# Optimization experiments

Measured on AMD Instinct MI355X. Metric: run time of the kernel, lower is better.

## Reference

```python
import jax, jax.numpy as jnp
import numpy as np

N_FREQ = 7  # freqs = 2**linspace(0, 6, 7) == 2**arange(7)
SKIP = (4,)


def nerf_encode(p):
    # nerfstudio NeRFEncoding with include_input=True, windows_param=None
    freqs = 2.0 ** jnp.arange(N_FREQ, dtype=p.dtype)          # [7]
    scaled = (2.0 * jnp.pi) * p                               # [N,3]
    s = (scaled[..., None] * freqs).reshape(p.shape[0], -1)   # [N,21]
    enc = jnp.sin(jnp.concatenate([s, s + 0.5 * jnp.pi], axis=-1))  # [N,42] = sin | cos
    return jnp.concatenate([enc, p], axis=-1)                 # [N,45]


def _hat_pt3d(w):
    # pytorch3d hat convention (transpose of the standard skew matrix)
    x, y, z = w[:, 0], w[:, 1], w[:, 2]
    o = jnp.zeros_like(x)
    return jnp.stack([
        jnp.stack([o, z, -y], -1),
        jnp.stack([-z, o, x], -1),
        jnp.stack([y, -x, o], -1)], -2)                       # [N,3,3]


def se3_exp_map_T(screw, eps=1e-4):
    # pytorch3d.transforms.se3_exp_map(screw).permute(0, 2, 1)
    v, w = screw[:, :3], screw[:, 3:]
    ang2 = jnp.clip(jnp.sum(w * w, axis=-1), eps, None)
    ang = jnp.sqrt(ang2)
    K = _hat_pt3d(w)
    KK = jnp.matmul(K, K)
    f1 = (jnp.sin(ang) / ang)[:, None, None]
    f2 = ((1.0 - jnp.cos(ang)) / ang2)[:, None, None]
    f3 = ((ang - jnp.sin(ang)) / (ang * ang2))[:, None, None]
    I = jnp.eye(3, dtype=screw.dtype)
    R = I + f1 * K + f2 * KK       # pytorch3d (row-vector) rotation
    V = I + f2 * K + f3 * KK
    T = jnp.einsum('nij,nj->ni', V, v)
    M = jnp.zeros((screw.shape[0], 4, 4), screw.dtype)
    M = M.at[:, :3, :3].set(jnp.swapaxes(R, -1, -2))  # transpose of [[R,0],[T,1]]
    M = M.at[:, :3, 3].set(T)
    M = M.at[:, 3, 3].set(1.0)
    return M


def mlp_stem(x, Ws, bs):
    inp = x
    n = len(Ws)
    for i in range(n):
        if i in SKIP:
            x = jnp.concatenate([inp, x], axis=-1)
        x = x @ Ws[i].T + bs[i]
        x = jax.nn.relu(x)  # hidden activation; i==n-1 is out_activation (also ReLU)
    return x


def setup_inputs() -> dict:
    key = jax.random.key(0)
    ks = jax.random.split(key, 16)
    N = 524288
    d = {
        'positions': jax.random.uniform(ks[0], (N, 3), jnp.float32),
        'directions': jax.random.normal(ks[1], (N, 3), jnp.float32),
        'warp_code': jax.random.normal(ks[2], (N, 8), jnp.float32),
    }
    fan_ins = [53, 128, 128, 128, 181, 128]
    for i, fi in enumerate(fan_ins):
        d[f'W{i}'] = jax.random.normal(ks[3 + i], (128, fi), jnp.float32) / np.sqrt(fi)
        d[f'b{i}'] = jnp.zeros((128,), jnp.float32)
    d['Wr'] = jax.random.normal(ks[10], (3, 128), jnp.float32) * 1e-5
    d['br'] = jnp.zeros((3,), jnp.float32)
    d['Wv'] = jax.random.normal(ks[11], (3, 128), jnp.float32) * 1e-5
    d['bv'] = jnp.zeros((3,), jnp.float32)
    return d


def reference(positions, directions, warp_code,
              W0, b0, W1, b1, W2, b2, W3, b3, W4, b4, W5, b5,
              Wr, br, Wv, bv):
    enc = nerf_encode(positions)                                  # [N,45]
    feat = mlp_stem(jnp.concatenate([enc, warp_code], axis=-1),
                    [W0, W1, W2, W3, W4, W5], [b0, b1, b2, b3, b4, b5])  # [N,128]
    r = feat @ Wr.T + br                                          # [N,3]
    v = feat @ Wv.T + bv                                          # [N,3]
    screw = jnp.concatenate([v, r], axis=-1)                      # [N,6]
    M = se3_exp_map_T(screw)                                      # [N,4,4]
    ph = jnp.concatenate([positions, jnp.ones_like(positions[:, :1])], axis=-1)
    wp_h = jnp.einsum('nij,nj->ni', M, ph)                        # [N,4]
    wp = wp_h[:, :3] / wp_h[:, 3:]
    wp = jnp.where(jnp.isnan(wp), positions, wp)
    rots = M[:, :3, :3]
    wd = jnp.einsum('nij,nj->ni', rots, directions)
    wd = jnp.where(jnp.isnan(wd), directions, wd)
    return wp, wd
```

## Files before the change

kernel.cpp:

```cpp
#include <hip/hip_runtime.h>
#include <hip/hip_bf16.h>
#include <math.h>


typedef __bf16 bf16x8 __attribute__((ext_vector_type(8)));
typedef float  f32x4  __attribute__((ext_vector_type(4)));

#define NROWS 524288
#define BROWS 128

#define P0 0
#define P1 8192
#define P2 24576
#define P3 40960
#define P4 57344
#define P5 81920
#define PH 98304
#define PTOT 100352

#define X0_OFF 0
#define XA_OFF 16384
#define SC_OFF 0
#define LDS_SZ 49152

__global__ void pack_w(const float* __restrict__ W0, const float* __restrict__ W1,
                       const float* __restrict__ W2, const float* __restrict__ W3,
                       const float* __restrict__ W4, const float* __restrict__ W5,
                       const float* __restrict__ Wr, const float* __restrict__ Wv,
                       __bf16* __restrict__ pk)
{
    int e = blockIdx.x * 256 + threadIdx.x;
    if (e >= PTOT) return;
    float val = 0.f;
    if (e >= PH) {
        int rem = e - PH;
        int s = rem >> 9, r3 = rem & 511, ln = r3 >> 3, j = r3 & 7;
        int col = ln & 15;
        int k = s * 32 + (ln >> 4) * 8 + j;
        if (col < 3)      val = Wv[col * 128 + k];
        else if (col < 6) val = Wr[(col - 3) * 128 + k];
        else              val = 0.f;
    } else {
        const float* W; int KS, base, fan;
        if (e < P1)      { W = W0; KS = 2; base = P0; fan = 53;  }
        else if (e < P2) { W = W1; KS = 4; base = P1; fan = 128; }
        else if (e < P3) { W = W2; KS = 4; base = P2; fan = 128; }
        else if (e < P4) { W = W3; KS = 4; base = P3; fan = 128; }
        else if (e < P5) { W = W4; KS = 6; base = P4; fan = 181; }
        else             { W = W5; KS = 4; base = P5; fan = 128; }
        int rem = e - base;
        int perf = KS * 512;
        int f = rem / perf, r2 = rem % perf;
        int s = r2 >> 9, r3 = r2 & 511, ln = r3 >> 3, j = r3 & 7;
        int col = f * 16 + (ln & 15);
        int k = s * 32 + (ln >> 4) * 8 + j;
        if (fan == 128)     val = W[col * 128 + k];
        else if (fan == 53) val = (k < 53) ? W[col * 53 + k] : 0.f;
        else {
            if (k < 53)      val = W[col * 181 + k];
            else if (k < 64) val = 0.f;
            else             val = W[col * 181 + (k - 11)];
        }
    }
    pk[e] = (__bf16)val;
}

__device__ __forceinline__ unsigned pack_bf16_2(float a, float b) {
    union { __bf16 h; unsigned short u; } x, y;
    x.h = (__bf16)a; y.h = (__bf16)b;
    return ((unsigned)y.u << 16) | (unsigned)x.u;
}

template<int KS, int SPLITS>
__device__ __forceinline__ void mlp_layer(unsigned char* smem,
    const __bf16* __restrict__ pkL, const float* __restrict__ bias,
    int inOff, int inStride, int outOff,
    int lane, int cl, int gp, int mfG, int nfG)
{
    const bf16x8* pW = (const bf16x8*)pkL;

    f32x4 acc[4][4];
    #pragma unroll
    for (int mf = 0; mf < 4; mf++) {
        f32x4 bb = *(const f32x4*)(bias + mfG * 64 + mf * 16 + gp * 4);
        #pragma unroll
        for (int nf = 0; nf < 4; nf++) acc[mf][nf] = bb;
    }

    bf16x8 Wf[2][4], Bf[2][4];
    auto loadW = [&](bf16x8* dst, int s) {
        #pragma unroll
        for (int mf = 0; mf < 4; mf++)
            dst[mf] = pW[((mfG * 4 + mf) * KS + s) * 64 + lane];
    };
    auto loadB = [&](bf16x8* dst, int s) {
        int base, stride, k0;
        if (s < SPLITS) { base = X0_OFF; stride = 128;      k0 = s * 32; }
        else            { base = inOff;  stride = inStride; k0 = (s - SPLITS) * 32; }
        int bc = 2 * k0 + 16 * gp;
        #pragma unroll
        for (int nf = 0; nf < 4; nf++) {
            int row = nfG * 64 + nf * 16 + cl;
            dst[nf] = *(const bf16x8*)(smem + base + row * stride
                                       + (bc ^ ((row & 7) << 4)));
        }
    };

    loadW(Wf[0], 0);
    loadB(Bf[0], 0);
    #pragma unroll
    for (int s = 0; s < KS; s++) {
        if (s + 1 < KS) { loadW(Wf[(s + 1) & 1], s + 1); loadB(Bf[(s + 1) & 1], s + 1); }
        #pragma unroll
        for (int mf = 0; mf < 4; mf++)
            #pragma unroll
            for (int nf = 0; nf < 4; nf++)
                acc[mf][nf] = __builtin_amdgcn_mfma_f32_16x16x32_bf16(
                    Wf[s & 1][mf], Bf[s & 1][nf], acc[mf][nf], 0, 0, 0);
    }

    __syncthreads();
    #pragma unroll
    for (int mf = 0; mf < 4; mf++)
        #pragma unroll
        for (int nf = 0; nf < 4; nf++) {
            int row = nfG * 64 + nf * 16 + cl;
            int bc  = 128 * mfG + 32 * mf + 8 * gp;
            f32x4 a = acc[mf][nf];
            uint2 w;
            w.x = pack_bf16_2(fmaxf(a[0], 0.f), fmaxf(a[1], 0.f));
            w.y = pack_bf16_2(fmaxf(a[2], 0.f), fmaxf(a[3], 0.f));
            *(uint2*)(smem + outOff + row * 256 + (bc ^ ((row & 7) << 4))) = w;
        }
    __syncthreads();
}

__global__ __launch_bounds__(256, 3)
void se3_fused(const float* __restrict__ pos, const float* __restrict__ dir,
               const float* __restrict__ wcode,
               const float* __restrict__ b0, const float* __restrict__ b1,
               const float* __restrict__ b2, const float* __restrict__ b3,
               const float* __restrict__ b4, const float* __restrict__ b5,
               const float* __restrict__ br, const float* __restrict__ bv,
               const __bf16* __restrict__ pk,
               float* __restrict__ out)
{
    __shared__ unsigned char smem[LDS_SZ];
    const int tid  = threadIdx.x;
    const int lane = tid & 63;
    const int cl   = lane & 15;
    const int gp   = lane >> 4;
    const int wid  = tid >> 6;
    const int mfG  = wid & 1;
    const int nfG  = wid >> 1;
    const int r0   = blockIdx.x * BROWS;

    {
        int row = tid >> 1, h = tid & 1;
        int g = r0 + row;
        float p3[3] = { pos[g*3+0], pos[g*3+1], pos[g*3+2] };
        unsigned char* base = smem + X0_OFF + row * 128;
        int sw = (row & 7) << 4;
        auto put = [&](int col, float v) {
            *(__bf16*)(base + ((col * 2) ^ sw)) = (__bf16)v;
        };
        if (h == 0) {
            #pragma unroll
            for (int a = 0; a < 3; a++)
                #pragma unroll
                for (int f = 0; f < 4; f++) {
                    float t = p3[a] * (float)(1 << f);
                    t -= floorf(t);
                    float ang = 6.283185307179586f * t;
                    put(a*7+f,      __sinf(ang));
                    put(21+a*7+f,   __cosf(ang));
                }
        } else {
            #pragma unroll
            for (int a = 0; a < 3; a++)
                #pragma unroll
                for (int f = 4; f < 7; f++) {
                    float t = p3[a] * (float)(1 << f);
                    t -= floorf(t);
                    float ang = 6.283185307179586f * t;
                    put(a*7+f,      __sinf(ang));
                    put(21+a*7+f,   __cosf(ang));
                }
            put(42, p3[0]); put(43, p3[1]); put(44, p3[2]);
            #pragma unroll
            for (int j = 0; j < 8; j++) put(45+j, wcode[g*8+j]);
            #pragma unroll
            for (int c = 53; c < 64; c++) put(c, 0.f);
        }
    }
    __syncthreads();

    mlp_layer<2,0>(smem, pk + P0, b0, X0_OFF, 128, XA_OFF, lane, cl, gp, mfG, nfG);
    mlp_layer<4,0>(smem, pk + P1, b1, XA_OFF, 256, XA_OFF, lane, cl, gp, mfG, nfG);
    mlp_layer<4,0>(smem, pk + P2, b2, XA_OFF, 256, XA_OFF, lane, cl, gp, mfG, nfG);
    mlp_layer<4,0>(smem, pk + P3, b3, XA_OFF, 256, XA_OFF, lane, cl, gp, mfG, nfG);
    mlp_layer<6,2>(smem, pk + P4, b4, XA_OFF, 256, XA_OFF, lane, cl, gp, mfG, nfG);
    mlp_layer<4,0>(smem, pk + P5, b5, XA_OFF, 256, XA_OFF, lane, cl, gp, mfG, nfG);

    if (mfG == 0) {
        const bf16x8* pW = (const bf16x8*)(pk + PH);
        f32x4 hb;
        #pragma unroll
        for (int r = 0; r < 4; r++) {
            int m = gp * 4 + r;
            hb[r] = (m < 3) ? bv[m] : ((m < 6) ? br[m - 3] : 0.f);
        }
        f32x4 hacc[4];
        #pragma unroll
        for (int nf = 0; nf < 4; nf++) hacc[nf] = hb;
        #pragma unroll
        for (int s = 0; s < 4; s++) {
            bf16x8 Wh = pW[s * 64 + lane];
            int bc = 64 * s + 16 * gp;
            #pragma unroll
            for (int nf = 0; nf < 4; nf++) {
                int row = nfG * 64 + nf * 16 + cl;
                bf16x8 B = *(const bf16x8*)(smem + XA_OFF + row * 256
                                            + (bc ^ ((row & 7) << 4)));
                hacc[nf] = __builtin_amdgcn_mfma_f32_16x16x32_bf16(Wh, B, hacc[nf], 0, 0, 0);
            }
        }
        #pragma unroll
        for (int nf = 0; nf < 4; nf++) {
            int row = nfG * 64 + nf * 16 + cl;
            if (gp == 0) {
                *(f32x4*)(smem + SC_OFF + row * 32) = hacc[nf];
            } else if (gp == 1) {
                *(float*)(smem + SC_OFF + row * 32 + 16) = hacc[nf][0];
                *(float*)(smem + SC_OFF + row * 32 + 20) = hacc[nf][1];
            }
        }
    }
    __syncthreads();

    if (tid < BROWS) {
        int row = tid, g = r0 + row;
        const float* sc = (const float*)(smem + SC_OFF + row * 32);
        float v0 = sc[0], v1 = sc[1], v2 = sc[2];
        float wx = sc[3], wy = sc[4], wz = sc[5];
        float ang2 = wx*wx + wy*wy + wz*wz;
        ang2 = fmaxf(ang2, 1e-4f);
        float ang = sqrtf(ang2);
        float sn = __sinf(ang), cs = __cosf(ang);
        float f1 = sn / ang;
        float f2 = (1.f - cs) / ang2;
        float f3 = (ang - sn) / (ang * ang2);
        float K[3][3] = {{0.f,  wz, -wy}, {-wz, 0.f,  wx}, { wy, -wx, 0.f}};
        float KK[3][3];
        #pragma unroll
        for (int i = 0; i < 3; i++)
            #pragma unroll
            for (int j = 0; j < 3; j++)
                KK[i][j] = K[i][0]*K[0][j] + K[i][1]*K[1][j] + K[i][2]*K[2][j];
        float R[3][3], V[3][3];
        #pragma unroll
        for (int i = 0; i < 3; i++)
            #pragma unroll
            for (int j = 0; j < 3; j++) {
                float id = (i == j) ? 1.f : 0.f;
                R[i][j] = id + f1 * K[i][j] + f2 * KK[i][j];
                V[i][j] = id + f2 * K[i][j] + f3 * KK[i][j];
            }
        float T0 = V[0][0]*v0 + V[0][1]*v1 + V[0][2]*v2;
        float T1 = V[1][0]*v0 + V[1][1]*v1 + V[1][2]*v2;
        float T2 = V[2][0]*v0 + V[2][1]*v1 + V[2][2]*v2;
        float px = pos[g*3+0], py = pos[g*3+1], pz = pos[g*3+2];
        float dx = dir[g*3+0], dy = dir[g*3+1], dz = dir[g*3+2];
        float wpx = R[0][0]*px + R[1][0]*py + R[2][0]*pz + T0;
        float wpy = R[0][1]*px + R[1][1]*py + R[2][1]*pz + T1;
        float wpz = R[0][2]*px + R[1][2]*py + R[2][2]*pz + T2;
        float wdx = R[0][0]*dx + R[1][0]*dy + R[2][0]*dz;
        float wdy = R[0][1]*dx + R[1][1]*dy + R[2][1]*dz;
        float wdz = R[0][2]*dx + R[1][2]*dy + R[2][2]*dz;
        wpx = (wpx != wpx) ? px : wpx;
        wpy = (wpy != wpy) ? py : wpy;
        wpz = (wpz != wpz) ? pz : wpz;
        wdx = (wdx != wdx) ? dx : wdx;
        wdy = (wdy != wdy) ? dy : wdy;
        wdz = (wdz != wdz) ? dz : wdz;
        out[g*3+0] = wpx; out[g*3+1] = wpy; out[g*3+2] = wpz;
        float* o2 = out + (size_t)NROWS * 3;
        o2[g*3+0] = wdx; o2[g*3+1] = wdy; o2[g*3+2] = wdz;
    }
}

extern "C" void kernel_launch(void* const* d_in, const int* in_sizes, int n_in,
                              void* d_out, int out_size, void* d_ws, size_t ws_size,
                              hipStream_t stream)
{
    const float* pos = (const float*)d_in[0];
    const float* dir = (const float*)d_in[1];
    const float* wc  = (const float*)d_in[2];
    const float* W0 = (const float*)d_in[3];  const float* b0 = (const float*)d_in[4];
    const float* W1 = (const float*)d_in[5];  const float* b1 = (const float*)d_in[6];
    const float* W2 = (const float*)d_in[7];  const float* b2 = (const float*)d_in[8];
    const float* W3 = (const float*)d_in[9];  const float* b3 = (const float*)d_in[10];
    const float* W4 = (const float*)d_in[11]; const float* b4 = (const float*)d_in[12];
    const float* W5 = (const float*)d_in[13]; const float* b5 = (const float*)d_in[14];
    const float* Wr = (const float*)d_in[15]; const float* br = (const float*)d_in[16];
    const float* Wv = (const float*)d_in[17]; const float* bv = (const float*)d_in[18];
    __bf16* pk = (__bf16*)d_ws;
    float* out = (float*)d_out;

    pack_w<<<(PTOT + 255) / 256, 256, 0, stream>>>(W0, W1, W2, W3, W4, W5, Wr, Wv, pk);
    se3_fused<<<NROWS / BROWS, 256, 0, stream>>>(pos, dir, wc,
                                                 b0, b1, b2, b3, b4, b5,
                                                 br, bv, pk, out);
}
```

Baseline: 221.9 us.

## Prefetch next layer's weights and bias into registers across MLP layers

Weights and bias for the next MLP layer are now loaded from global memory into a persistent register array during the epilogue of the current layer, so their latency overlaps the LDS writeback and barrier instead of stalling the start of each layer. The input encoding now builds bf16 values in registers and writes them as packed 16-byte LDS stores, and the final barrier only waits on LDS traffic (lgkmcnt) so outstanding global prefetches are not drained. The weight-packing kernel is restructured with templated helpers, and the head weights are hoisted. Holding a 4x4 bf16x8 weight array raises register pressure and may hurt occupancy under the 3-blocks launch bound.

```diff
diff --git a/kernel.cpp b/kernel.cpp
--- a/kernel.cpp
+++ b/kernel.cpp
@@ -23,6 +23,21 @@
 #define SC_OFF 0
 #define LDS_SZ 49152
 
+template<int KS, int FAN>
+__device__ __forceinline__ float pack_val(const float* __restrict__ W, int idx)
+{
+    int f  = idx / (KS * 512);
+    int r2 = idx % (KS * 512);
+    int s  = r2 >> 9, r3 = r2 & 511, ln = r3 >> 3, j = r3 & 7;
+    int col = f * 16 + (ln & 15);
+    int k   = s * 32 + (ln >> 4) * 8 + j;
+    if (FAN == 128) return W[col * 128 + k];
+    if (FAN == 53)  return (k < 53) ? W[col * 53 + k] : 0.f;
+    if (k < 53)  return W[col * 181 + k];
+    if (k < 64)  return 0.f;
+    return W[col * 181 + (k - 11)];
+}
+
 __global__ void pack_w(const float* __restrict__ W0, const float* __restrict__ W1,
                        const float* __restrict__ W2, const float* __restrict__ W3,
                        const float* __restrict__ W4, const float* __restrict__ W5,
@@ -31,7 +46,7 @@
 {
     int e = blockIdx.x * 256 + threadIdx.x;
     if (e >= PTOT) return;
-    float val = 0.f;
+    float val;
     if (e >= PH) {
         int rem = e - PH;
         int s = rem >> 9, r3 = rem & 511, ln = r3 >> 3, j = r3 & 7;
@@ -40,28 +55,13 @@
         if (col < 3)      val = Wv[col * 128 + k];
         else if (col < 6) val = Wr[(col - 3) * 128 + k];
         else              val = 0.f;
-    } else {
-        const float* W; int KS, base, fan;
-        if (e < P1)      { W = W0; KS = 2; base = P0; fan = 53;  }
-        else if (e < P2) { W = W1; KS = 4; base = P1; fan = 128; }
-        else if (e < P3) { W = W2; KS = 4; base = P2; fan = 128; }
-        else if (e < P4) { W = W3; KS = 4; base = P3; fan = 128; }
-        else if (e < P5) { W = W4; KS = 6; base = P4; fan = 181; }
-        else             { W = W5; KS = 4; base = P5; fan = 128; }
-        int rem = e - base;
-        int perf = KS * 512;
-        int f = rem / perf, r2 = rem % perf;
-        int s = r2 >> 9, r3 = r2 & 511, ln = r3 >> 3, j = r3 & 7;
-        int col = f * 16 + (ln & 15);
-        int k = s * 32 + (ln >> 4) * 8 + j;
-        if (fan == 128)     val = W[col * 128 + k];
-        else if (fan == 53) val = (k < 53) ? W[col * 53 + k] : 0.f;
-        else {
-            if (k < 53)      val = W[col * 181 + k];
-            else if (k < 64) val = 0.f;
-            else             val = W[col * 181 + (k - 11)];
-        }
-    }
+    }
+    else if (e < P1) val = pack_val<2, 53 >(W0, e - P0);
+    else if (e < P2) val = pack_val<4, 128>(W1, e - P1);
+    else if (e < P3) val = pack_val<4, 128>(W2, e - P2);
+    else if (e < P4) val = pack_val<4, 128>(W3, e - P3);
+    else if (e < P5) val = pack_val<6, 181>(W4, e - P4);
+    else             val = pack_val<4, 128>(W5, e - P5);
     pk[e] = (__bf16)val;
 }
 
@@ -71,28 +71,21 @@
     return ((unsigned)y.u << 16) | (unsigned)x.u;
 }
 
-template<int KS, int SPLITS>
+template<int KS, int SPLITS, int KSN>
 __device__ __forceinline__ void mlp_layer(unsigned char* smem,
-    const __bf16* __restrict__ pkL, const float* __restrict__ bias,
+    bf16x8 (&W)[4][4], f32x4 (&Bias)[4],
+    const __bf16* __restrict__ pkCur, const __bf16* __restrict__ pkNext,
+    const float* __restrict__ biasNext,
     int inOff, int inStride, int outOff,
     int lane, int cl, int gp, int mfG, int nfG)
 {
-    const bf16x8* pW = (const bf16x8*)pkL;
-
     f32x4 acc[4][4];
     #pragma unroll
-    for (int mf = 0; mf < 4; mf++) {
-        f32x4 bb = *(const f32x4*)(bias + mfG * 64 + mf * 16 + gp * 4);
-        #pragma unroll
-        for (int nf = 0; nf < 4; nf++) acc[mf][nf] = bb;
-    }
-
-    bf16x8 Wf[2][4], Bf[2][4];
-    auto loadW = [&](bf16x8* dst, int s) {
-        #pragma unroll
-        for (int mf = 0; mf < 4; mf++)
-            dst[mf] = pW[((mfG * 4 + mf) * KS + s) * 64 + lane];
-    };
+    for (int mf = 0; mf < 4; mf++)
+        #pragma unroll
+        for (int nf = 0; nf < 4; nf++) acc[mf][nf] = Bias[mf];
+
+    bf16x8 Bf[2][4];
     auto loadB = [&](bf16x8* dst, int s) {
         int base, stride, k0;
         if (s < SPLITS) { base = X0_OFF; stride = 128;      k0 = s * 32; }
@@ -106,20 +99,41 @@
         }
     };
 
-    loadW(Wf[0], 0);
     loadB(Bf[0], 0);
     #pragma unroll
     for (int s = 0; s < KS; s++) {
-        if (s + 1 < KS) { loadW(Wf[(s + 1) & 1], s + 1); loadB(Bf[(s + 1) & 1], s + 1); }
+        if (s + 1 < KS) loadB(Bf[(s + 1) & 1], s + 1);
         #pragma unroll
         for (int mf = 0; mf < 4; mf++)
             #pragma unroll
             for (int nf = 0; nf < 4; nf++)
                 acc[mf][nf] = __builtin_amdgcn_mfma_f32_16x16x32_bf16(
-                    Wf[s & 1][mf], Bf[s & 1][nf], acc[mf][nf], 0, 0, 0);
+                    W[s & 3][mf], Bf[s & 1][nf], acc[mf][nf], 0, 0, 0);
+        if constexpr (KS > 4) {
+            if (s + 4 < KS) {
+                const bf16x8* pC = (const bf16x8*)pkCur;
+                #pragma unroll
+                for (int mf = 0; mf < 4; mf++)
+                    W[(s + 4) & 3][mf] = pC[((mfG * 4 + mf) * KS + (s + 4)) * 64 + lane];
+            }
+        }
     }
 
     __syncthreads();
+
+    if constexpr (KSN > 0) {
+        constexpr int PF = (KSN > 4) ? 4 : KSN;
+        const bf16x8* pN = (const bf16x8*)pkNext;
+        #pragma unroll
+        for (int s = 0; s < PF; s++)
+            #pragma unroll
+            for (int mf = 0; mf < 4; mf++)
+                W[s][mf] = pN[((mfG * 4 + mf) * KSN + s) * 64 + lane];
+        #pragma unroll
+        for (int mf = 0; mf < 4; mf++)
+            Bias[mf] = *(const f32x4*)(biasNext + mfG * 64 + mf * 16 + gp * 4);
+    }
+
     #pragma unroll
     for (int mf = 0; mf < 4; mf++)
         #pragma unroll
@@ -132,7 +146,10 @@
             w.y = pack_bf16_2(fmaxf(a[2], 0.f), fmaxf(a[3], 0.f));
             *(uint2*)(smem + outOff + row * 256 + (bc ^ ((row & 7) << 4))) = w;
         }
-    __syncthreads();
+
+    asm volatile("s_waitcnt lgkmcnt(0)" ::: "memory");
+    __builtin_amdgcn_s_barrier();
+    asm volatile("" ::: "memory");
 }
 
 __global__ __launch_bounds__(256, 3)
@@ -155,55 +172,83 @@
     const int nfG  = wid >> 1;
     const int r0   = blockIdx.x * BROWS;
 
+    bf16x8 W[4][4];
+    f32x4  Bias[4];
+    {
+        const bf16x8* p0v = (const bf16x8*)(pk + P0);
+        #pragma unroll
+        for (int s = 0; s < 2; s++)
+            #pragma unroll
+            for (int mf = 0; mf < 4; mf++)
+                W[s][mf] = p0v[((mfG * 4 + mf) * 2 + s) * 64 + lane];
+        #pragma unroll
+        for (int mf = 0; mf < 4; mf++)
+            Bias[mf] = *(const f32x4*)(b0 + mfG * 64 + mf * 16 + gp * 4);
+    }
+
     {
         int row = tid >> 1, h = tid & 1;
         int g = r0 + row;
-        float p3[3] = { pos[g*3+0], pos[g*3+1], pos[g*3+2] };
+        float p0 = pos[g*3+0], p1 = pos[g*3+1], p2 = pos[g*3+2];
+        float vals[32];
+        if (h == 0) {
+            #pragma unroll
+            for (int j = 0; j < 21; j++) {
+                float p = (j < 7) ? p0 : (j < 14 ? p1 : p2);
+                float t = p * (float)(1 << (j % 7));
+                t -= floorf(t);
+                vals[j] = __sinf(6.283185307179586f * t);
+            }
+            #pragma unroll
+            for (int j = 21; j < 32; j++) {
+                int idx = j - 21;
+                float p = (idx < 7) ? p0 : (idx < 14 ? p1 : p2);
+                float t = p * (float)(1 << (idx % 7));
+                t -= floorf(t);
+                vals[j] = __cosf(6.283185307179586f * t);
+            }
+        } else {
+            #pragma unroll
+            for (int j = 0; j < 10; j++) {
+                int idx = 11 + j;
+                float p = (idx < 14) ? p1 : p2;
+                float t = p * (float)(1 << (idx % 7));
+                t -= floorf(t);
+                vals[j] = __cosf(6.283185307179586f * t);
+            }
+            vals[10] = p0; vals[11] = p1; vals[12] = p2;
+            const float4* wc4 = (const float4*)(wcode + (size_t)g * 8);
+            float4 wa = wc4[0], wb = wc4[1];
+            vals[13] = wa.x; vals[14] = wa.y; vals[15] = wa.z; vals[16] = wa.w;
+            vals[17] = wb.x; vals[18] = wb.y; vals[19] = wb.z; vals[20] = wb.w;
+            #pragma unroll
+            for (int j = 21; j < 32; j++) vals[j] = 0.f;
+        }
+        unsigned pkd[16];
+        #pragma unroll
+        for (int i = 0; i < 16; i++) pkd[i] = pack_bf16_2(vals[2*i], vals[2*i+1]);
         unsigned char* base = smem + X0_OFF + row * 128;
         int sw = (row & 7) << 4;
-        auto put = [&](int col, float v) {
-            *(__bf16*)(base + ((col * 2) ^ sw)) = (__bf16)v;
-        };
-        if (h == 0) {
-            #pragma unroll
-            for (int a = 0; a < 3; a++)
-                #pragma unroll
-                for (int f = 0; f < 4; f++) {
-                    float t = p3[a] * (float)(1 << f);
-                    t -= floorf(t);
-                    float ang = 6.283185307179586f * t;
-                    put(a*7+f,      __sinf(ang));
-                    put(21+a*7+f,   __cosf(ang));
-                }
-        } else {
-            #pragma unroll
-            for (int a = 0; a < 3; a++)
-                #pragma unroll
-                for (int f = 4; f < 7; f++) {
-                    float t = p3[a] * (float)(1 << f);
-                    t -= floorf(t);
-                    float ang = 6.283185307179586f * t;
-                    put(a*7+f,      __sinf(ang));
-                    put(21+a*7+f,   __cosf(ang));
-                }
-            put(42, p3[0]); put(43, p3[1]); put(44, p3[2]);
-            #pragma unroll
-            for (int j = 0; j < 8; j++) put(45+j, wcode[g*8+j]);
-            #pragma unroll
-            for (int c = 53; c < 64; c++) put(c, 0.f);
+        #pragma unroll
+        for (int c = 0; c < 4; c++) {
+            uint4 w; w.x = pkd[4*c]; w.y = pkd[4*c+1]; w.z = pkd[4*c+2]; w.w = pkd[4*c+3];
+            *(uint4*)(base + ((64 * h + 16 * c) ^ sw)) = w;
         }
     }
     __syncthreads();
 
-    mlp_layer<2,0>(smem, pk + P0, b0, X0_OFF, 128, XA_OFF, lane, cl, gp, mfG, nfG);
-    mlp_layer<4,0>(smem, pk + P1, b1, XA_OFF, 256, XA_OFF, lane, cl, gp, mfG, nfG);
-    mlp_layer<4,0>(smem, pk + P2, b2, XA_OFF, 256, XA_OFF, lane, cl, gp, mfG, nfG);
-    mlp_layer<4,0>(smem, pk + P3, b3, XA_OFF, 256, XA_OFF, lane, cl, gp, mfG, nfG);
-    mlp_layer<6,2>(smem, pk + P4, b4, XA_OFF, 256, XA_OFF, lane, cl, gp, mfG, nfG);
-    mlp_layer<4,0>(smem, pk + P5, b5, XA_OFF, 256, XA_OFF, lane, cl, gp, mfG, nfG);
+    mlp_layer<2,0,4>(smem, W, Bias, pk+P0, pk+P1, b1, X0_OFF, 128, XA_OFF, lane, cl, gp, mfG, nfG);
+    mlp_layer<4,0,4>(smem, W, Bias, pk+P1, pk+P2, b2, XA_OFF, 256, XA_OFF, lane, cl, gp, mfG, nfG);
+    mlp_layer<4,0,4>(smem, W, Bias, pk+P2, pk+P3, b3, XA_OFF, 256, XA_OFF, lane, cl, gp, mfG, nfG);
+    mlp_layer<4,0,6>(smem, W, Bias, pk+P3, pk+P4, b4, XA_OFF, 256, XA_OFF, lane, cl, gp, mfG, nfG);
+    mlp_layer<6,2,4>(smem, W, Bias, pk+P4, pk+P5, b5, XA_OFF, 256, XA_OFF, lane, cl, gp, mfG, nfG);
+    mlp_layer<4,0,0>(smem, W, Bias, pk+P5, nullptr, nullptr, XA_OFF, 256, XA_OFF, lane, cl, gp, mfG, nfG);
 
     if (mfG == 0) {
         const bf16x8* pW = (const bf16x8*)(pk + PH);
+        bf16x8 Wh[4];
+        #pragma unroll
+        for (int s = 0; s < 4; s++) Wh[s] = pW[s * 64 + lane];
         f32x4 hb;
         #pragma unroll
         for (int r = 0; r < 4; r++) {
@@ -215,14 +260,13 @@
         for (int nf = 0; nf < 4; nf++) hacc[nf] = hb;
         #pragma unroll
         for (int s = 0; s < 4; s++) {
-            bf16x8 Wh = pW[s * 64 + lane];
             int bc = 64 * s + 16 * gp;
             #pragma unroll
             for (int nf = 0; nf < 4; nf++) {
                 int row = nfG * 64 + nf * 16 + cl;
                 bf16x8 B = *(const bf16x8*)(smem + XA_OFF + row * 256
                                             + (bc ^ ((row & 7) << 4)));
-                hacc[nf] = __builtin_amdgcn_mfma_f32_16x16x32_bf16(Wh, B, hacc[nf], 0, 0, 0);
+                hacc[nf] = __builtin_amdgcn_mfma_f32_16x16x32_bf16(Wh[s], B, hacc[nf], 0, 0, 0);
             }
         }
         #pragma unroll
```

Result: no change. 224.7 us (+1.3%).
